# Kernel tuning notes

Measured on AMD Instinct MI355X. Metric: run time of the kernel, lower is better.

The kernel has to match this reference:

```python
import jax, jax.numpy as jnp
import numpy as np

N_EDGES = 1600000
N_NODES = 50000
D_FEAT = 48


def setup_inputs() -> dict:
    key = jax.random.key(0)
    k1, k2, k3 = jax.random.split(key, 3)
    a = jax.random.normal(k1, (N_EDGES,), dtype=jnp.float32)
    ft = jax.random.normal(k2, (N_EDGES, D_FEAT), dtype=jnp.float32)
    segment_ids = jnp.sort(jax.random.randint(k3, (N_EDGES,), 0, N_NODES, dtype=jnp.int32))
    return {"a": a, "ft": ft, "segment_ids": segment_ids, "n_nodes": N_NODES}


def reference(a, ft, segment_ids, n_nodes):
    # Segment softmax over incoming edges of each destination node
    # (the torch module does softmax over the stacked neighbor-message axis).
    seg_max = jax.ops.segment_max(a, segment_ids, num_segments=n_nodes)  # [N]
    seg_max = jax.lax.stop_gradient(seg_max)  # stabilizer only, grad-neutral
    ex = jnp.exp(a - seg_max[segment_ids])                               # [E]
    denom = jax.ops.segment_sum(ex, segment_ids, num_segments=n_nodes)  # [N]
    e = ex / denom[segment_ids]                                         # [E]
    # Weighted sum of neighbor features per node: sum_e e * ft  -> [N, D]
    out = jax.ops.segment_sum(e[:, None] * ft, segment_ids, num_segments=n_nodes)
    return out
```

## Files before the change

kernel.cpp:

```cpp
#include <hip/hip_runtime.h>
#include <cfloat>
#include <cstdint>

#define D_FEAT 48

__global__ void build_rowptr(const int* __restrict__ seg, int E, int N,
                             int* __restrict__ row_ptr) {
    int e = blockIdx.x * blockDim.x + threadIdx.x;
    if (e >= E) return;
    int s  = seg[e];
    int sp = (e == 0) ? -1 : seg[e - 1];
    for (int n = sp + 1; n <= s; ++n) row_ptr[n] = e;
    if (e == E - 1) {
        for (int n = s + 1; n <= N; ++n) row_ptr[n] = E;
    }
}

__global__ __launch_bounds__(256) void gat_reduce(
    const float* __restrict__ a, const float* __restrict__ ft,
    const int* __restrict__ row_ptr, float* __restrict__ out, int N)
{
    int lane = threadIdx.x & 63;
    int n = blockIdx.x * 4 + (threadIdx.x >> 6);
    if (n >= N) return;

    int lo  = row_ptr[n];
    int hi  = row_ptr[n + 1];
    int cnt = hi - lo;

    int m    = lane % 12;
    int ecls = lane / 12;

    if (cnt <= 0) {
        if (lane < 12) {
            float4 z = {0.f, 0.f, 0.f, 0.f};
            *(float4*)(out + (size_t)n * D_FEAT + 4 * lane) = z;
        }
        return;
    }

    float mx = -FLT_MAX;
    for (int i = lane; i < cnt; i += 64) mx = fmaxf(mx, a[lo + i]);
    #pragma unroll
    for (int o = 32; o > 0; o >>= 1) mx = fmaxf(mx, __shfl_xor(mx, o, 64));

    float s = 0.0f;
    for (int i = lane; i < cnt; i += 64) s += __expf(a[lo + i] - mx);
    #pragma unroll
    for (int o = 32; o > 0; o >>= 1) s += __shfl_xor(s, o, 64);
    float inv = 1.0f / s;

    float4 acc = {0.f, 0.f, 0.f, 0.f};
    if (lane < 48) {
        const float* base = ft + (size_t)lo * D_FEAT + 4 * m;
        const float* ap   = a + lo;
        int ngroups = (cnt + 3) >> 2;
        for (int g = 0; g < ngroups; g += 4) {
            float4 f[4];
            #pragma unroll
            for (int k = 0; k < 4; ++k) {
                int e  = (g + k) * 4 + ecls;
                int ec = min(e, cnt - 1);
                f[k] = *(const float4*)(base + (size_t)ec * D_FEAT);
            }
            float w[4];
            #pragma unroll
            for (int k = 0; k < 4; ++k) {
                int e  = (g + k) * 4 + ecls;
                int ec = min(e, cnt - 1);
                float av = ap[ec];
                w[k] = (e < cnt) ? __expf(av - mx) : 0.0f;
            }
            #pragma unroll
            for (int k = 0; k < 4; ++k) {
                acc.x = fmaf(w[k], f[k].x, acc.x);
                acc.y = fmaf(w[k], f[k].y, acc.y);
                acc.z = fmaf(w[k], f[k].z, acc.z);
                acc.w = fmaf(w[k], f[k].w, acc.w);
            }
        }
    }

    float4 t;
    t.x = __shfl(acc.x, lane + 24, 64); t.y = __shfl(acc.y, lane + 24, 64);
    t.z = __shfl(acc.z, lane + 24, 64); t.w = __shfl(acc.w, lane + 24, 64);
    acc.x += t.x; acc.y += t.y; acc.z += t.z; acc.w += t.w;
    t.x = __shfl(acc.x, lane + 12, 64); t.y = __shfl(acc.y, lane + 12, 64);
    t.z = __shfl(acc.z, lane + 12, 64); t.w = __shfl(acc.w, lane + 12, 64);
    acc.x += t.x; acc.y += t.y; acc.z += t.z; acc.w += t.w;

    if (lane < 12) {
        float4 r = {acc.x * inv, acc.y * inv, acc.z * inv, acc.w * inv};
        *(float4*)(out + (size_t)n * D_FEAT + 4 * lane) = r;
    }
}

extern "C" void kernel_launch(void* const* d_in, const int* in_sizes, int n_in,
                              void* d_out, int out_size, void* d_ws, size_t ws_size,
                              hipStream_t stream) {
    const float* a   = (const float*)d_in[0];
    const float* ft  = (const float*)d_in[1];
    const int*   seg = (const int*)d_in[2];
    int E = in_sizes[0];
    int N = out_size / D_FEAT;

    int* row_ptr = (int*)d_ws;

    build_rowptr<<<(E + 255) / 256, 256, 0, stream>>>(seg, E, N, row_ptr);
    gat_reduce<<<(N + 3) / 4, 256, 0, stream>>>(a, ft, row_ptr, (float*)d_out, N);
}
```

Baseline: 422.8 us.

## Precompute exp weights and segment denominators in a separate atomic-scan kernel

Adds a kernel that computes exp(a) per edge without subtracting the segment max, and sums each segment's denominator with a wave-level segmented scan plus atomics. The accumulation kernel then reads the precomputed weights and divides by the denominator, which removes the per-node max and sum passes. The accumulation loop is also unrolled to 8 groups, and feature loads and output stores become nontemporal. Dropping the max subtraction risks overflow for large logits, adds an extra launch and an E-sized workspace array, and makes the float atomic summation order nondeterministic.

Measured after the change: 405.4 us. 1.04x faster.

```diff
diff --git a/kernel.cpp b/kernel.cpp
--- a/kernel.cpp
+++ b/kernel.cpp
@@ -4,9 +4,12 @@
 
 #define D_FEAT 48
 
-__global__ void build_rowptr(const int* __restrict__ seg, int E, int N,
-                             int* __restrict__ row_ptr) {
+typedef float f4 __attribute__((ext_vector_type(4)));
+
+__global__ void k0_rowptr_init(const int* __restrict__ seg, int E, int N,
+                               int* __restrict__ row_ptr, float* __restrict__ den) {
     int e = blockIdx.x * blockDim.x + threadIdx.x;
+    if (e < N) den[e] = 0.0f;
     if (e >= E) return;
     int s  = seg[e];
     int sp = (e == 0) ? -1 : seg[e - 1];
@@ -16,9 +19,31 @@
     }
 }
 
-__global__ __launch_bounds__(256) void gat_reduce(
-    const float* __restrict__ a, const float* __restrict__ ft,
-    const int* __restrict__ row_ptr, float* __restrict__ out, int N)
+__global__ __launch_bounds__(256) void k1_weights(
+    const float* __restrict__ a, const int* __restrict__ seg, int E,
+    float* __restrict__ ex, float* __restrict__ den)
+{
+    int e    = blockIdx.x * blockDim.x + threadIdx.x;
+    int lane = threadIdx.x & 63;
+    bool valid = e < E;
+    int   k = valid ? seg[e] : 0x7fffffff;
+    float v = valid ? __expf(a[e]) : 0.0f;
+    if (valid) ex[e] = v;
+    #pragma unroll
+    for (int s = 1; s < 64; s <<= 1) {
+        float pv = __shfl_up(v, s, 64);
+        int   pk = __shfl_up(k, s, 64);
+        if (lane >= s && pk == k) v += pv;
+    }
+    int nk = __shfl_down(k, 1, 64);
+    bool last = (lane == 63) || (nk != k);
+    if (valid && last) atomicAdd(&den[k], v);
+}
+
+__global__ __launch_bounds__(256) void k2_accum(
+    const float* __restrict__ ft, const float* __restrict__ ex,
+    const int* __restrict__ row_ptr, const float* __restrict__ den,
+    float* __restrict__ out, int N)
 {
     int lane = threadIdx.x & 63;
     int n = blockIdx.x * 4 + (threadIdx.x >> 6);
@@ -28,51 +53,41 @@
     int hi  = row_ptr[n + 1];
     int cnt = hi - lo;
 
-    int m    = lane % 12;
-    int ecls = lane / 12;
-
     if (cnt <= 0) {
         if (lane < 12) {
-            float4 z = {0.f, 0.f, 0.f, 0.f};
-            *(float4*)(out + (size_t)n * D_FEAT + 4 * lane) = z;
+            f4 z = {0.f, 0.f, 0.f, 0.f};
+            __builtin_nontemporal_store(z, (f4*)(out + (size_t)n * D_FEAT + 4 * lane));
         }
         return;
     }
+    float inv = 1.0f / den[n];
 
-    float mx = -FLT_MAX;
-    for (int i = lane; i < cnt; i += 64) mx = fmaxf(mx, a[lo + i]);
-    #pragma unroll
-    for (int o = 32; o > 0; o >>= 1) mx = fmaxf(mx, __shfl_xor(mx, o, 64));
+    int m    = lane % 12;
+    int ecls = lane / 12;
+    f4 acc = {0.f, 0.f, 0.f, 0.f};
 
-    float s = 0.0f;
-    for (int i = lane; i < cnt; i += 64) s += __expf(a[lo + i] - mx);
-    #pragma unroll
-    for (int o = 32; o > 0; o >>= 1) s += __shfl_xor(s, o, 64);
-    float inv = 1.0f / s;
-
-    float4 acc = {0.f, 0.f, 0.f, 0.f};
     if (lane < 48) {
         const float* base = ft + (size_t)lo * D_FEAT + 4 * m;
-        const float* ap   = a + lo;
+        const float* wp   = ex + lo;
         int ngroups = (cnt + 3) >> 2;
-        for (int g = 0; g < ngroups; g += 4) {
-            float4 f[4];
+        for (int g = 0; g < ngroups; g += 8) {
+            f4 f[8];
             #pragma unroll
-            for (int k = 0; k < 4; ++k) {
+            for (int k = 0; k < 8; ++k) {
                 int e  = (g + k) * 4 + ecls;
                 int ec = min(e, cnt - 1);
-                f[k] = *(const float4*)(base + (size_t)ec * D_FEAT);
+                f[k] = __builtin_nontemporal_load((const f4*)(base + (size_t)ec * D_FEAT));
             }
-            float w[4];
+            float w[8];
             #pragma unroll
-            for (int k = 0; k < 4; ++k) {
+            for (int k = 0; k < 8; ++k) {
                 int e  = (g + k) * 4 + ecls;
                 int ec = min(e, cnt - 1);
-                float av = ap[ec];
-                w[k] = (e < cnt) ? __expf(av - mx) : 0.0f;
+                float wv = wp[ec];
+                w[k] = (e < cnt) ? wv : 0.0f;
             }
             #pragma unroll
-            for (int k = 0; k < 4; ++k) {
+            for (int k = 0; k < 8; ++k) {
                 acc.x = fmaf(w[k], f[k].x, acc.x);
                 acc.y = fmaf(w[k], f[k].y, acc.y);
                 acc.z = fmaf(w[k], f[k].z, acc.z);
@@ -81,7 +96,7 @@
         }
     }
 
-    float4 t;
+    f4 t;
     t.x = __shfl(acc.x, lane + 24, 64); t.y = __shfl(acc.y, lane + 24, 64);
     t.z = __shfl(acc.z, lane + 24, 64); t.w = __shfl(acc.w, lane + 24, 64);
     acc.x += t.x; acc.y += t.y; acc.z += t.z; acc.w += t.w;
@@ -90,8 +105,8 @@
     acc.x += t.x; acc.y += t.y; acc.z += t.z; acc.w += t.w;
 
     if (lane < 12) {
-        float4 r = {acc.x * inv, acc.y * inv, acc.z * inv, acc.w * inv};
-        *(float4*)(out + (size_t)n * D_FEAT + 4 * lane) = r;
+        f4 r = {acc.x * inv, acc.y * inv, acc.z * inv, acc.w * inv};
+        __builtin_nontemporal_store(r, (f4*)(out + (size_t)n * D_FEAT + 4 * lane));
     }
 }
 
@@ -104,8 +119,15 @@
     int E = in_sizes[0];
     int N = out_size / D_FEAT;
 
-    int* row_ptr = (int*)d_ws;
+    char* wsb = (char*)d_ws;
+    int*   row_ptr = (int*)wsb;
+    size_t off = (((size_t)(N + 1) * 4) + 255) & ~(size_t)255;
+    float* den = (float*)(wsb + off);
+    off = (off + (size_t)N * 4 + 255) & ~(size_t)255;
+    float* ex  = (float*)(wsb + off);
 
-    build_rowptr<<<(E + 255) / 256, 256, 0, stream>>>(seg, E, N, row_ptr);
-    gat_reduce<<<(N + 3) / 4, 256, 0, stream>>>(a, ft, row_ptr, (float*)d_out, N);
+    int gridE = (E + 255) / 256;
+    k0_rowptr_init<<<gridE, 256, 0, stream>>>(seg, E, N, row_ptr, den);
+    k1_weights   <<<gridE, 256, 0, stream>>>(a, seg, E, ex, den);
+    k2_accum     <<<(N + 3) / 4, 256, 0, stream>>>(ft, ex, row_ptr, den, (float*)d_out, N);
 }
```
